# Kernel optimization log

Measured on AMD Instinct MI355X. Metric: run time of the kernel, lower is better.

## Reference

```python
import jax, jax.numpy as jnp
import numpy as np

N = 20000      # nodes
E = 320000     # edges (before self-loops)
G = 64         # graphs in batch
IN = 128       # input_dim
HID = 64       # hidden_dim
H1 = 4         # heads of conv1
NEG_SLOPE = 0.2


def setup_inputs() -> dict:
    key = jax.random.key(0)
    ks = jax.random.split(key, 14)
    x = jax.random.normal(ks[0], (N, IN), jnp.float32)
    edge_index = jax.random.randint(ks[1], (2, E), 0, N, dtype=jnp.int32)
    batch = jnp.sort(jax.random.randint(ks[2], (N,), 0, G, dtype=jnp.int32))
    # conv1: in=IN, out=HID, heads=4, concat
    W1 = jax.random.normal(ks[3], (IN, H1 * HID), jnp.float32) / np.float32(np.sqrt(IN))
    a_src1 = jax.random.normal(ks[4], (H1, HID), jnp.float32) / np.float32(np.sqrt(HID))
    a_dst1 = jax.random.normal(ks[5], (H1, HID), jnp.float32) / np.float32(np.sqrt(HID))
    b1 = jnp.zeros((H1 * HID,), jnp.float32)
    # conv2: in=4*HID, out=HID, heads=1
    W2 = jax.random.normal(ks[6], (H1 * HID, HID), jnp.float32) / np.float32(np.sqrt(H1 * HID))
    a_src2 = jax.random.normal(ks[7], (1, HID), jnp.float32) / np.float32(np.sqrt(HID))
    a_dst2 = jax.random.normal(ks[8], (1, HID), jnp.float32) / np.float32(np.sqrt(HID))
    b2 = jnp.zeros((HID,), jnp.float32)
    # final linear HID -> 1
    W_lin = jax.random.normal(ks[9], (HID, 1), jnp.float32) / np.float32(np.sqrt(HID))
    b_lin = jnp.zeros((1,), jnp.float32)
    return dict(x=x, edge_index=edge_index, batch=batch,
                W1=W1, a_src1=a_src1, a_dst1=a_dst1, b1=b1,
                W2=W2, a_src2=a_src2, a_dst2=a_dst2, b2=b2,
                W_lin=W_lin, b_lin=b_lin)


def gat_conv(x, src, dst, W, a_src, a_dst, b, heads, out_ch, n_nodes):
    """PyG-style GATConv (v1), concat=True, with self-loops already in src/dst."""
    h = (x @ W).reshape(n_nodes, heads, out_ch)          # [N,H,C]
    s = jnp.einsum('nhc,hc->nh', h, a_src)               # [N,H] per-node src score
    d = jnp.einsum('nhc,hc->nh', h, a_dst)               # [N,H] per-node dst score
    logits = jax.nn.leaky_relu(s[src] + d[dst], NEG_SLOPE)   # [Etot,H]
    # segment softmax over incoming edges of each destination node
    m = jax.ops.segment_max(logits, dst, num_segments=n_nodes)
    m = jnp.where(jnp.isfinite(m), m, 0.0)
    e = jnp.exp(logits - m[dst])                         # [Etot,H]
    denom = jax.ops.segment_sum(e, dst, num_segments=n_nodes)
    alpha = e / denom[dst]                               # every node has a self-loop -> denom>0
    out = jax.ops.segment_sum(alpha[:, :, None] * h[src], dst, num_segments=n_nodes)  # [N,H,C]
    return out.reshape(n_nodes, heads * out_ch) + b


def reference(x, edge_index, batch,
              W1, a_src1, a_dst1, b1,
              W2, a_src2, a_dst2, b2,
              W_lin, b_lin):
    n = x.shape[0]
    loop = jnp.arange(n, dtype=edge_index.dtype)
    src = jnp.concatenate([edge_index[0], loop])   # add self-loops (PyG default)
    dst = jnp.concatenate([edge_index[1], loop])
    h = jax.nn.elu(gat_conv(x, src, dst, W1, a_src1, a_dst1, b1, H1, HID, n))
    h = jax.nn.elu(gat_conv(h, src, dst, W2, a_src2, a_dst2, b2, 1, HID, n))
    # global mean pool over graphs
    sums = jax.ops.segment_sum(h, batch, num_segments=G)                 # [G,HID]
    cnt = jax.ops.segment_sum(jnp.ones((n,), h.dtype), batch, num_segments=G)
    pooled = sums / jnp.maximum(cnt, 1.0)[:, None]
    return (pooled @ W_lin + b_lin).squeeze(-1)    # [G]
```

## Files before the change

kernel.cpp:

```cpp
#include <hip/hip_runtime.h>
#include <cstdint>


__device__ __forceinline__ float leaky02(float x) { return x > 0.f ? x : 0.2f * x; }
__device__ __forceinline__ float eluf(float x) { return x > 0.f ? x : expm1f(x); }

template <int H>
__device__ __forceinline__ void sgemm_scores_body(
    const float* __restrict__ A, const float* __restrict__ B, float* __restrict__ C,
    int M, int K, const float* __restrict__ asrc, const float* __restrict__ adst,
    float* __restrict__ sT, float* __restrict__ dS, float* __restrict__ wself,
    int bx, int by, float* As_, float* Bs_) {
    constexpr int Nc = H * 64;
    float (*As)[68] = (float(*)[68])As_;
    float (*Bs)[68] = (float(*)[68])Bs_;
    const int tid = threadIdx.x;
    const int bm = bx * 64, bn = by * 64;
    const int ty = tid >> 4, tx = tid & 15;
    float acc[4][4] = {};
    for (int k0 = 0; k0 < K; k0 += 32) {
#pragma unroll
        for (int i = 0; i < 8; i++) {
            int idx = tid + i * 256;
            int m = idx >> 5, kk = idx & 31;
            int gm = bm + m;
            if (gm >= M) gm = 0;
            As[kk][m] = A[(size_t)gm * K + k0 + kk];
        }
#pragma unroll
        for (int i = 0; i < 8; i++) {
            int idx = tid + i * 256;
            int kk = idx >> 6, n = idx & 63;
            Bs[kk][n] = B[(size_t)(k0 + kk) * Nc + bn + n];
        }
        __syncthreads();
#pragma unroll
        for (int kk = 0; kk < 32; kk++) {
            float4 a4 = *(const float4*)&As[kk][ty * 4];
            float4 b4 = *(const float4*)&Bs[kk][tx * 4];
            float av[4] = {a4.x, a4.y, a4.z, a4.w};
            float bv[4] = {b4.x, b4.y, b4.z, b4.w};
#pragma unroll
            for (int r = 0; r < 4; r++)
#pragma unroll
                for (int c2 = 0; c2 < 4; c2++) acc[r][c2] += av[r] * bv[c2];
        }
        __syncthreads();
    }
    const int h = by;
    float sr[4], dr[4];
#pragma unroll
    for (int r = 0; r < 4; r++) {
        float s = 0.f, d = 0.f;
#pragma unroll
        for (int c2 = 0; c2 < 4; c2++) {
            float hv = acc[r][c2];
            s += hv * asrc[h * 64 + tx * 4 + c2];
            d += hv * adst[h * 64 + tx * 4 + c2];
        }
        sr[r] = s;
        dr[r] = d;
    }
#pragma unroll
    for (int off = 1; off <= 8; off <<= 1) {
#pragma unroll
        for (int r = 0; r < 4; r++) {
            sr[r] += __shfl_xor(sr[r], off);
            dr[r] += __shfl_xor(dr[r], off);
        }
    }
#pragma unroll
    for (int r = 0; r < 4; r++) {
        int gm = bm + ty * 4 + r;
        if (gm < M) {
            float4 o = make_float4(acc[r][0], acc[r][1], acc[r][2], acc[r][3]);
            *(float4*)&C[(size_t)gm * Nc + bn + tx * 4] = o;
            if (tx == 0) {
                sT[(size_t)h * M + gm] = sr[r];
                dS[gm * H + h] = dr[r];
                wself[gm * H + h] = __expf(leaky02(sr[r] + dr[r]));
            }
        }
    }
}

__global__ __launch_bounds__(256) void fused_sgemm4_init_kernel(
    const float* __restrict__ A, const float* __restrict__ B, float* __restrict__ C,
    int M, int K, const float* __restrict__ asrc, const float* __restrict__ adst,
    float* __restrict__ sT, float* __restrict__ dS, float* __restrict__ wself,
    int GBX, int GB1, int4* __restrict__ initp, int colN4, int totN4) {
    __shared__ __align__(16) float As_[32][68];
    __shared__ __align__(16) float Bs_[32][68];
    const int b = blockIdx.x;
    if (b >= GB1) {
        int i = (b - GB1) * 256 + threadIdx.x;
        if (i < totN4)
            initp[i] = (i < colN4) ? make_int4(-1, -1, -1, -1) : make_int4(0, 0, 0, 0);
        return;
    }
    sgemm_scores_body<4>(A, B, C, M, K, asrc, adst, sT, dS, wself,
                         b % GBX, b / GBX, &As_[0][0], &Bs_[0][0]);
}

__global__ __launch_bounds__(256) void sgemm_scores1_kernel(
    const float* __restrict__ A, const float* __restrict__ B, float* __restrict__ C,
    int M, int K, const float* __restrict__ asrc, const float* __restrict__ adst,
    float* __restrict__ sT, float* __restrict__ dS, float* __restrict__ wself) {
    __shared__ __align__(16) float As_[32][68];
    __shared__ __align__(16) float Bs_[32][68];
    sgemm_scores_body<1>(A, B, C, M, K, asrc, adst, sT, dS, wself,
                         blockIdx.x, 0, &As_[0][0], &Bs_[0][0]);
}

__global__ void fill_kernel(const int* __restrict__ src, const int* __restrict__ dst,
                            int* __restrict__ cursor, int* __restrict__ col, int E) {
    int e = blockIdx.x * blockDim.x + threadIdx.x;
    if (e >= E) return;
    int d = dst[e];
    int p = atomicAdd(&cursor[d], 1);
    if (p < 64) col[(d << 6) + p] = src[e];
}

__global__ __launch_bounds__(256) void gat_agg4_kernel(
    const float* __restrict__ hbuf, const float* __restrict__ sT,
    const float* __restrict__ dsc, const float* __restrict__ wself,
    const int* __restrict__ cursor, const int* __restrict__ col,
    const float* __restrict__ bias, float* __restrict__ out, int N) {
    const int slice = blockIdx.x & 7;
    const int lane = threadIdx.x & 63;
    const int cq = lane & 7;
    const int vidx = (blockIdx.x >> 3) * 32 + (threadIdx.x >> 6) * 8 + (lane >> 3);
    const bool valid = vidx < N;
    const int v = min(vidx, N - 1);
    const int deg = min(cursor[v], 64);
    const int base = v << 6;
    const int cbase = slice * 32 + cq * 4;
    const int hh = slice >> 1;
    const float* __restrict__ sTh = sT + (size_t)hh * N;
    const char* __restrict__ hb = (const char*)hbuf + ((size_t)cbase << 2);
    const float dvh = dsc[v * 4 + hh];
    float w = wself[v * 4 + hh];
    float den = w;
    float4 hv = *(const float4*)(hb + ((unsigned)v << 10));
    float4 acc = make_float4(w * hv.x, w * hv.y, w * hv.z, w * hv.w);
    const int end8 = (deg + 7) & ~7;
    for (int j = 0; j < end8; j += 8) {
        int4 a = *(const int4*)&col[base + j];
        int4 b = *(const int4*)&col[base + j + 4];
        unsigned o0 = (unsigned)max(a.x, 0) << 10, o1 = (unsigned)max(a.y, 0) << 10;
        unsigned o2 = (unsigned)max(a.z, 0) << 10, o3 = (unsigned)max(a.w, 0) << 10;
        unsigned o4 = (unsigned)max(b.x, 0) << 10, o5 = (unsigned)max(b.y, 0) << 10;
        unsigned o6 = (unsigned)max(b.z, 0) << 10, o7 = (unsigned)max(b.w, 0) << 10;
        float4 h0 = *(const float4*)(hb + o0);
        float4 h1 = *(const float4*)(hb + o1);
        float4 h2 = *(const float4*)(hb + o2);
        float4 h3 = *(const float4*)(hb + o3);
        float4 h4 = *(const float4*)(hb + o4);
        float4 h5 = *(const float4*)(hb + o5);
        float4 h6 = *(const float4*)(hb + o6);
        float4 h7 = *(const float4*)(hb + o7);
        float w0 = (a.x >= 0) ? __expf(leaky02(sTh[o0 >> 10] + dvh)) : 0.f;
        float w1 = (a.y >= 0) ? __expf(leaky02(sTh[o1 >> 10] + dvh)) : 0.f;
        float w2 = (a.z >= 0) ? __expf(leaky02(sTh[o2 >> 10] + dvh)) : 0.f;
        float w3 = (a.w >= 0) ? __expf(leaky02(sTh[o3 >> 10] + dvh)) : 0.f;
        float w4 = (b.x >= 0) ? __expf(leaky02(sTh[o4 >> 10] + dvh)) : 0.f;
        float w5 = (b.y >= 0) ? __expf(leaky02(sTh[o5 >> 10] + dvh)) : 0.f;
        float w6 = (b.z >= 0) ? __expf(leaky02(sTh[o6 >> 10] + dvh)) : 0.f;
        float w7 = (b.w >= 0) ? __expf(leaky02(sTh[o7 >> 10] + dvh)) : 0.f;
        den += w0 + w1 + w2 + w3 + w4 + w5 + w6 + w7;
        acc.x += w0 * h0.x + w1 * h1.x + w2 * h2.x + w3 * h3.x;
        acc.y += w0 * h0.y + w1 * h1.y + w2 * h2.y + w3 * h3.y;
        acc.z += w0 * h0.z + w1 * h1.z + w2 * h2.z + w3 * h3.z;
        acc.w += w0 * h0.w + w1 * h1.w + w2 * h2.w + w3 * h3.w;
        acc.x += w4 * h4.x + w5 * h5.x + w6 * h6.x + w7 * h7.x;
        acc.y += w4 * h4.y + w5 * h5.y + w6 * h6.y + w7 * h7.y;
        acc.z += w4 * h4.z + w5 * h5.z + w6 * h6.z + w7 * h7.z;
        acc.w += w4 * h4.w + w5 * h5.w + w6 * h6.w + w7 * h7.w;
    }
    if (valid) {
        float4 b4 = *(const float4*)&bias[cbase];
        float inv = 1.f / den;
        float4 r;
        r.x = eluf(acc.x * inv + b4.x);
        r.y = eluf(acc.y * inv + b4.y);
        r.z = eluf(acc.z * inv + b4.z);
        r.w = eluf(acc.w * inv + b4.w);
        *(float4*)&out[(size_t)v * 256 + cbase] = r;
    }
}

__global__ __launch_bounds__(256) void gat_agg1_kernel(
    const float* __restrict__ hbuf, const float* __restrict__ sT,
    const float* __restrict__ dsc, const float* __restrict__ wself,
    const int* __restrict__ cursor, const int* __restrict__ col,
    const float* __restrict__ bias, const float* __restrict__ Wlin,
    float* __restrict__ pn0, float* __restrict__ pn1, int N) {
    const int slice = blockIdx.x & 1;
    const int lane = threadIdx.x & 63;
    const int cq = lane & 7;
    const int vidx = (blockIdx.x >> 1) * 32 + (threadIdx.x >> 6) * 8 + (lane >> 3);
    const bool valid = vidx < N;
    const int v = min(vidx, N - 1);
    const int deg = min(cursor[v], 64);
    const int base = v << 6;
    const int cbase = slice * 32 + cq * 4;
    const char* __restrict__ hb = (const char*)hbuf + ((size_t)cbase << 2);
    const float dv = dsc[v];
    float w = wself[v];
    float den = w;
    float4 hv = *(const float4*)(hb + ((unsigned)v << 8));
    float4 acc = make_float4(w * hv.x, w * hv.y, w * hv.z, w * hv.w);
    const int end8 = (deg + 7) & ~7;
    for (int j = 0; j < end8; j += 8) {
        int4 a = *(const int4*)&col[base + j];
        int4 b = *(const int4*)&col[base + j + 4];
        unsigned i0 = (unsigned)max(a.x, 0), i1 = (unsigned)max(a.y, 0);
        unsigned i2 = (unsigned)max(a.z, 0), i3 = (unsigned)max(a.w, 0);
        unsigned i4 = (unsigned)max(b.x, 0), i5 = (unsigned)max(b.y, 0);
        unsigned i6 = (unsigned)max(b.z, 0), i7 = (unsigned)max(b.w, 0);
        float4 h0 = *(const float4*)(hb + (i0 << 8));
        float4 h1 = *(const float4*)(hb + (i1 << 8));
        float4 h2 = *(const float4*)(hb + (i2 << 8));
        float4 h3 = *(const float4*)(hb + (i3 << 8));
        float4 h4 = *(const float4*)(hb + (i4 << 8));
        float4 h5 = *(const float4*)(hb + (i5 << 8));
        float4 h6 = *(const float4*)(hb + (i6 << 8));
        float4 h7 = *(const float4*)(hb + (i7 << 8));
        float w0 = (a.x >= 0) ? __expf(leaky02(sT[i0] + dv)) : 0.f;
        float w1 = (a.y >= 0) ? __expf(leaky02(sT[i1] + dv)) : 0.f;
        float w2 = (a.z >= 0) ? __expf(leaky02(sT[i2] + dv)) : 0.f;
        float w3 = (a.w >= 0) ? __expf(leaky02(sT[i3] + dv)) : 0.f;
        float w4 = (b.x >= 0) ? __expf(leaky02(sT[i4] + dv)) : 0.f;
        float w5 = (b.y >= 0) ? __expf(leaky02(sT[i5] + dv)) : 0.f;
        float w6 = (b.z >= 0) ? __expf(leaky02(sT[i6] + dv)) : 0.f;
        float w7 = (b.w >= 0) ? __expf(leaky02(sT[i7] + dv)) : 0.f;
        den += w0 + w1 + w2 + w3 + w4 + w5 + w6 + w7;
        acc.x += w0 * h0.x + w1 * h1.x + w2 * h2.x + w3 * h3.x;
        acc.y += w0 * h0.y + w1 * h1.y + w2 * h2.y + w3 * h3.y;
        acc.z += w0 * h0.z + w1 * h1.z + w2 * h2.z + w3 * h3.z;
        acc.w += w0 * h0.w + w1 * h1.w + w2 * h2.w + w3 * h3.w;
        acc.x += w4 * h4.x + w5 * h5.x + w6 * h6.x + w7 * h7.x;
        acc.y += w4 * h4.y + w5 * h5.y + w6 * h6.y + w7 * h7.y;
        acc.z += w4 * h4.z + w5 * h5.z + w6 * h6.z + w7 * h7.z;
        acc.w += w4 * h4.w + w5 * h5.w + w6 * h6.w + w7 * h7.w;
    }
    float4 b4 = *(const float4*)&bias[cbase];
    float4 wl = *(const float4*)&Wlin[cbase];
    float inv = 1.f / den;
    float p = eluf(acc.x * inv + b4.x) * wl.x + eluf(acc.y * inv + b4.y) * wl.y +
              eluf(acc.z * inv + b4.z) * wl.z + eluf(acc.w * inv + b4.w) * wl.w;
    p += __shfl_xor(p, 1);
    p += __shfl_xor(p, 2);
    p += __shfl_xor(p, 4);
    if (valid && cq == 0) (slice ? pn1 : pn0)[v] = p;
}

__global__ __launch_bounds__(64) void finalize_kernel(const float* __restrict__ pn0,
                                                      const float* __restrict__ pn1,
                                                      const int* __restrict__ batch,
                                                      const float* __restrict__ blin,
                                                      float* __restrict__ outp, int N, int G) {
    const int g = blockIdx.x;
    const int lane = threadIdx.x;
    int lo = 0, hi = N;
    while (lo < hi) { int mid = (lo + hi) >> 1; if (batch[mid] < g) lo = mid + 1; else hi = mid; }
    int lo2 = lo, hi2 = N;
    while (lo2 < hi2) { int mid = (lo2 + hi2) >> 1; if (batch[mid] < g + 1) lo2 = mid + 1; else hi2 = mid; }
    float s = 0.f;
    for (int i = lo + lane; i < hi2; i += 64) s += pn0[i] + pn1[i];
#pragma unroll
    for (int off = 32; off > 0; off >>= 1) s += __shfl_xor(s, off);
    if (lane == 0) {
        float cnt = (float)(hi2 - lo);
        outp[g] = s / fmaxf(cnt, 1.f) + blin[0];
    }
}

extern "C" void kernel_launch(void* const* d_in, const int* in_sizes, int n_in,
                              void* d_out, int out_size, void* d_ws, size_t ws_size,
                              hipStream_t stream) {
    const float* x      = (const float*)d_in[0];
    const int*   ei     = (const int*)d_in[1];
    const int*   batch  = (const int*)d_in[2];
    const float* W1     = (const float*)d_in[3];
    const float* a_src1 = (const float*)d_in[4];
    const float* a_dst1 = (const float*)d_in[5];
    const float* b1     = (const float*)d_in[6];
    const float* W2     = (const float*)d_in[7];
    const float* a_src2 = (const float*)d_in[8];
    const float* a_dst2 = (const float*)d_in[9];
    const float* b2     = (const float*)d_in[10];
    const float* Wlin   = (const float*)d_in[11];
    const float* blin   = (const float*)d_in[12];

    const int N = in_sizes[2];
    const int E = in_sizes[1] / 2;
    const int G = out_size;
    const int* src = ei;
    const int* dst = ei + E;

    char* ws = (char*)d_ws;
    size_t off = 0;
    auto carve = [&](size_t bytes) -> char* {
        char* p = ws + off;
        off = (off + bytes + 255) & ~(size_t)255;
        return p;
    };
    float* h1      = (float*)carve((size_t)N * 256 * 4);
    float* out1    = (float*)carve((size_t)N * 256 * 4);
    float* sT1     = (float*)carve((size_t)4 * N * 4);
    float* d1      = (float*)carve((size_t)N * 4 * 4);
    float* wself1  = (float*)carve((size_t)N * 4 * 4);
    float* sT2     = (float*)carve((size_t)N * 4);
    float* d2      = (float*)carve((size_t)N * 4);
    float* wself2  = (float*)carve((size_t)N * 4);
    int*   colcur  = (int*)carve(((size_t)N * 64 + N) * 4);
    float* pn0     = (float*)carve((size_t)N * 4);
    float* pn1     = (float*)carve((size_t)N * 4);
    float* h2      = h1;
    int* col = colcur;
    int* cursor = colcur + (size_t)N * 64;

    const int GBX = (N + 63) / 64;
    const int GB1 = GBX * 4;
    const int totN4 = (N * 64 + N) / 4;
    const int colN4 = N * 16;
    const int GBI = (totN4 + 255) / 256;

    fused_sgemm4_init_kernel<<<GB1 + GBI, 256, 0, stream>>>(
        x, W1, h1, N, 128, a_src1, a_dst1, sT1, d1, wself1,
        GBX, GB1, (int4*)colcur, colN4, totN4);
    fill_kernel<<<(E + 255) / 256, 256, 0, stream>>>(src, dst, cursor, col, E);

    const int nodeGroups32 = (N + 31) / 32;
    gat_agg4_kernel<<<8 * nodeGroups32, 256, 0, stream>>>(h1, sT1, d1, wself1, cursor, col,
                                                          b1, out1, N);
    sgemm_scores1_kernel<<<dim3(GBX, 1), 256, 0, stream>>>(
        out1, W2, h2, N, 256, a_src2, a_dst2, sT2, d2, wself2);
    gat_agg1_kernel<<<2 * nodeGroups32, 256, 0, stream>>>(h2, sT2, d2, wself2, cursor, col,
                                                          b2, Wlin, pn0, pn1, N);
    finalize_kernel<<<G, 64, 0, stream>>>(pn0, pn1, batch, blin, (float*)d_out, N, G);
}
```

Measured before the change: 135.7 us.

## Precompute per-edge layer-1 attention weights in CSR fill kernel

The adjacency-fill kernel now also computes exp(leaky_relu(s_src+d_dst)) for all four heads of every edge and stores it in a slot-aligned, per-head buffer. The layer-1 aggregation then reads these weights contiguously instead of gathering source scores and recomputing exponentials in every channel slice. Source scores are stored node-major so the fill kernel can read them as float4. Both aggregation loops are also reduced from 8-way to 4-way unrolling. The trade-off is an extra scattered write of weights and a larger workspace, plus less memory-level parallelism in the inner loops.

New measurement: 143.2 us. +5.5%, slower.

```diff
diff --git a/kernel.cpp b/kernel.cpp
--- a/kernel.cpp
+++ b/kernel.cpp
@@ -9,7 +9,7 @@
 __device__ __forceinline__ void sgemm_scores_body(
     const float* __restrict__ A, const float* __restrict__ B, float* __restrict__ C,
     int M, int K, const float* __restrict__ asrc, const float* __restrict__ adst,
-    float* __restrict__ sT, float* __restrict__ dS, float* __restrict__ wself,
+    float* __restrict__ sS, float* __restrict__ dS, float* __restrict__ wself,
     int bx, int by, float* As_, float* Bs_) {
     constexpr int Nc = H * 64;
     float (*As)[68] = (float(*)[68])As_;
@@ -76,7 +76,7 @@
             float4 o = make_float4(acc[r][0], acc[r][1], acc[r][2], acc[r][3]);
             *(float4*)&C[(size_t)gm * Nc + bn + tx * 4] = o;
             if (tx == 0) {
-                sT[(size_t)h * M + gm] = sr[r];
+                sS[gm * H + h] = sr[r];
                 dS[gm * H + h] = dr[r];
                 wself[gm * H + h] = __expf(leaky02(sr[r] + dr[r]));
             }
@@ -87,7 +87,7 @@
 __global__ __launch_bounds__(256) void fused_sgemm4_init_kernel(
     const float* __restrict__ A, const float* __restrict__ B, float* __restrict__ C,
     int M, int K, const float* __restrict__ asrc, const float* __restrict__ adst,
-    float* __restrict__ sT, float* __restrict__ dS, float* __restrict__ wself,
+    float* __restrict__ sS, float* __restrict__ dS, float* __restrict__ wself,
     int GBX, int GB1, int4* __restrict__ initp, int colN4, int totN4) {
     __shared__ __align__(16) float As_[32][68];
     __shared__ __align__(16) float Bs_[32][68];
@@ -98,34 +98,44 @@
             initp[i] = (i < colN4) ? make_int4(-1, -1, -1, -1) : make_int4(0, 0, 0, 0);
         return;
     }
-    sgemm_scores_body<4>(A, B, C, M, K, asrc, adst, sT, dS, wself,
+    sgemm_scores_body<4>(A, B, C, M, K, asrc, adst, sS, dS, wself,
                          b % GBX, b / GBX, &As_[0][0], &Bs_[0][0]);
 }
 
 __global__ __launch_bounds__(256) void sgemm_scores1_kernel(
     const float* __restrict__ A, const float* __restrict__ B, float* __restrict__ C,
     int M, int K, const float* __restrict__ asrc, const float* __restrict__ adst,
-    float* __restrict__ sT, float* __restrict__ dS, float* __restrict__ wself) {
+    float* __restrict__ sS, float* __restrict__ dS, float* __restrict__ wself) {
     __shared__ __align__(16) float As_[32][68];
     __shared__ __align__(16) float Bs_[32][68];
-    sgemm_scores_body<1>(A, B, C, M, K, asrc, adst, sT, dS, wself,
+    sgemm_scores_body<1>(A, B, C, M, K, asrc, adst, sS, dS, wself,
                          blockIdx.x, 0, &As_[0][0], &Bs_[0][0]);
 }
 
-__global__ void fill_kernel(const int* __restrict__ src, const int* __restrict__ dst,
-                            int* __restrict__ cursor, int* __restrict__ col, int E) {
+__global__ void fill_w4_kernel(const int* __restrict__ src, const int* __restrict__ dst,
+                               int* __restrict__ cursor, int* __restrict__ col,
+                               const float* __restrict__ s1, const float* __restrict__ d1,
+                               float* __restrict__ w, int E, int N64) {
     int e = blockIdx.x * blockDim.x + threadIdx.x;
     if (e >= E) return;
-    int d = dst[e];
+    int s = src[e], d = dst[e];
     int p = atomicAdd(&cursor[d], 1);
-    if (p < 64) col[(d << 6) + p] = src[e];
+    if (p >= 64) return;
+    int slot = (d << 6) + p;
+    col[slot] = s;
+    float4 sv = *(const float4*)&s1[s * 4];
+    float4 dv = *(const float4*)&d1[d * 4];
+    w[slot]            = __expf(leaky02(sv.x + dv.x));
+    w[N64 + slot]      = __expf(leaky02(sv.y + dv.y));
+    w[2 * N64 + slot]  = __expf(leaky02(sv.z + dv.z));
+    w[3 * N64 + slot]  = __expf(leaky02(sv.w + dv.w));
 }
 
 __global__ __launch_bounds__(256) void gat_agg4_kernel(
-    const float* __restrict__ hbuf, const float* __restrict__ sT,
-    const float* __restrict__ dsc, const float* __restrict__ wself,
-    const int* __restrict__ cursor, const int* __restrict__ col,
-    const float* __restrict__ bias, float* __restrict__ out, int N) {
+    const float* __restrict__ hbuf, const float* __restrict__ w,
+    const float* __restrict__ wself, const int* __restrict__ cursor,
+    const int* __restrict__ col, const float* __restrict__ bias,
+    float* __restrict__ out, int N) {
     const int slice = blockIdx.x & 7;
     const int lane = threadIdx.x & 63;
     const int cq = lane & 7;
@@ -136,46 +146,31 @@
     const int base = v << 6;
     const int cbase = slice * 32 + cq * 4;
     const int hh = slice >> 1;
-    const float* __restrict__ sTh = sT + (size_t)hh * N;
+    const float* __restrict__ wp = w + (size_t)hh * (N << 6);
     const char* __restrict__ hb = (const char*)hbuf + ((size_t)cbase << 2);
-    const float dvh = dsc[v * 4 + hh];
-    float w = wself[v * 4 + hh];
-    float den = w;
+    float ws = wself[v * 4 + hh];
+    float den = ws;
     float4 hv = *(const float4*)(hb + ((unsigned)v << 10));
-    float4 acc = make_float4(w * hv.x, w * hv.y, w * hv.z, w * hv.w);
-    const int end8 = (deg + 7) & ~7;
-    for (int j = 0; j < end8; j += 8) {
-        int4 a = *(const int4*)&col[base + j];
-        int4 b = *(const int4*)&col[base + j + 4];
-        unsigned o0 = (unsigned)max(a.x, 0) << 10, o1 = (unsigned)max(a.y, 0) << 10;
-        unsigned o2 = (unsigned)max(a.z, 0) << 10, o3 = (unsigned)max(a.w, 0) << 10;
-        unsigned o4 = (unsigned)max(b.x, 0) << 10, o5 = (unsigned)max(b.y, 0) << 10;
-        unsigned o6 = (unsigned)max(b.z, 0) << 10, o7 = (unsigned)max(b.w, 0) << 10;
+    float4 acc = make_float4(ws * hv.x, ws * hv.y, ws * hv.z, ws * hv.w);
+    const int end4 = (deg + 3) & ~3;
+    for (int j = 0; j < end4; j += 4) {
+        int4 c4 = *(const int4*)&col[base + j];
+        float4 w4 = *(const float4*)&wp[base + j];
+        unsigned o0 = (unsigned)max(c4.x, 0) << 10, o1 = (unsigned)max(c4.y, 0) << 10;
+        unsigned o2 = (unsigned)max(c4.z, 0) << 10, o3 = (unsigned)max(c4.w, 0) << 10;
         float4 h0 = *(const float4*)(hb + o0);
         float4 h1 = *(const float4*)(hb + o1);
         float4 h2 = *(const float4*)(hb + o2);
         float4 h3 = *(const float4*)(hb + o3);
-        float4 h4 = *(const float4*)(hb + o4);
-        float4 h5 = *(const float4*)(hb + o5);
-        float4 h6 = *(const float4*)(hb + o6);
-        float4 h7 = *(const float4*)(hb + o7);
-        float w0 = (a.x >= 0) ? __expf(leaky02(sTh[o0 >> 10] + dvh)) : 0.f;
-        float w1 = (a.y >= 0) ? __expf(leaky02(sTh[o1 >> 10] + dvh)) : 0.f;
-        float w2 = (a.z >= 0) ? __expf(leaky02(sTh[o2 >> 10] + dvh)) : 0.f;
-        float w3 = (a.w >= 0) ? __expf(leaky02(sTh[o3 >> 10] + dvh)) : 0.f;
-        float w4 = (b.x >= 0) ? __expf(leaky02(sTh[o4 >> 10] + dvh)) : 0.f;
-        float w5 = (b.y >= 0) ? __expf(leaky02(sTh[o5 >> 10] + dvh)) : 0.f;
-        float w6 = (b.z >= 0) ? __expf(leaky02(sTh[o6 >> 10] + dvh)) : 0.f;
-        float w7 = (b.w >= 0) ? __expf(leaky02(sTh[o7 >> 10] + dvh)) : 0.f;
-        den += w0 + w1 + w2 + w3 + w4 + w5 + w6 + w7;
+        float w0 = (c4.x >= 0) ? w4.x : 0.f;
+        float w1 = (c4.y >= 0) ? w4.y : 0.f;
+        float w2 = (c4.z >= 0) ? w4.z : 0.f;
+        float w3 = (c4.w >= 0) ? w4.w : 0.f;
+        den += w0 + w1 + w2 + w3;
         acc.x += w0 * h0.x + w1 * h1.x + w2 * h2.x + w3 * h3.x;
         acc.y += w0 * h0.y + w1 * h1.y + w2 * h2.y + w3 * h3.y;
         acc.z += w0 * h0.z + w1 * h1.z + w2 * h2.z + w3 * h3.z;
         acc.w += w0 * h0.w + w1 * h1.w + w2 * h2.w + w3 * h3.w;
-        acc.x += w4 * h4.x + w5 * h5.x + w6 * h6.x + w7 * h7.x;
-        acc.y += w4 * h4.y + w5 * h5.y + w6 * h6.y + w7 * h7.y;
-        acc.z += w4 * h4.z + w5 * h5.z + w6 * h6.z + w7 * h7.z;
-        acc.w += w4 * h4.w + w5 * h5.w + w6 * h6.w + w7 * h7.w;
     }
     if (valid) {
         float4 b4 = *(const float4*)&bias[cbase];
@@ -190,7 +185,7 @@
 }
 
 __global__ __launch_bounds__(256) void gat_agg1_kernel(
-    const float* __restrict__ hbuf, const float* __restrict__ sT,
+    const float* __restrict__ hbuf, const float* __restrict__ s2,
     const float* __restrict__ dsc, const float* __restrict__ wself,
     const int* __restrict__ cursor, const int* __restrict__ col,
     const float* __restrict__ bias, const float* __restrict__ Wlin,
@@ -206,43 +201,28 @@
     const int cbase = slice * 32 + cq * 4;
     const char* __restrict__ hb = (const char*)hbuf + ((size_t)cbase << 2);
     const float dv = dsc[v];
-    float w = wself[v];
-    float den = w;
+    float ws = wself[v];
+    float den = ws;
     float4 hv = *(const float4*)(hb + ((unsigned)v << 8));
-    float4 acc = make_float4(w * hv.x, w * hv.y, w * hv.z, w * hv.w);
-    const int end8 = (deg + 7) & ~7;
-    for (int j = 0; j < end8; j += 8) {
-        int4 a = *(const int4*)&col[base + j];
-        int4 b = *(const int4*)&col[base + j + 4];
-        unsigned i0 = (unsigned)max(a.x, 0), i1 = (unsigned)max(a.y, 0);
-        unsigned i2 = (unsigned)max(a.z, 0), i3 = (unsigned)max(a.w, 0);
-        unsigned i4 = (unsigned)max(b.x, 0), i5 = (unsigned)max(b.y, 0);
-        unsigned i6 = (unsigned)max(b.z, 0), i7 = (unsigned)max(b.w, 0);
+    float4 acc = make_float4(ws * hv.x, ws * hv.y, ws * hv.z, ws * hv.w);
+    const int end4 = (deg + 3) & ~3;
+    for (int j = 0; j < end4; j += 4) {
+        int4 c4 = *(const int4*)&col[base + j];
+        unsigned i0 = (unsigned)max(c4.x, 0), i1 = (unsigned)max(c4.y, 0);
+        unsigned i2 = (unsigned)max(c4.z, 0), i3 = (unsigned)max(c4.w, 0);
         float4 h0 = *(const float4*)(hb + (i0 << 8));
         float4 h1 = *(const float4*)(hb + (i1 << 8));
         float4 h2 = *(const float4*)(hb + (i2 << 8));
         float4 h3 = *(const float4*)(hb + (i3 << 8));
-        float4 h4 = *(const float4*)(hb + (i4 << 8));
-        float4 h5 = *(const float4*)(hb + (i5 << 8));
-        float4 h6 = *(const float4*)(hb + (i6 << 8));
-        float4 h7 = *(const float4*)(hb + (i7 << 8));
-        float w0 = (a.x >= 0) ? __expf(leaky02(sT[i0] + dv)) : 0.f;
-        float w1 = (a.y >= 0) ? __expf(leaky02(sT[i1] + dv)) : 0.f;
-        float w2 = (a.z >= 0) ? __expf(leaky02(sT[i2] + dv)) : 0.f;
-        float w3 = (a.w >= 0) ? __expf(leaky02(sT[i3] + dv)) : 0.f;
-        float w4 = (b.x >= 0) ? __expf(leaky02(sT[i4] + dv)) : 0.f;
-        float w5 = (b.y >= 0) ? __expf(leaky02(sT[i5] + dv)) : 0.f;
-        float w6 = (b.z >= 0) ? __expf(leaky02(sT[i6] + dv)) : 0.f;
-        float w7 = (b.w >= 0) ? __expf(leaky02(sT[i7] + dv)) : 0.f;
-        den += w0 + w1 + w2 + w3 + w4 + w5 + w6 + w7;
+        float w0 = (c4.x >= 0) ? __expf(leaky02(s2[i0] + dv)) : 0.f;
+        float w1 = (c4.y >= 0) ? __expf(leaky02(s2[i1] + dv)) : 0.f;
+        float w2 = (c4.z >= 0) ? __expf(leaky02(s2[i2] + dv)) : 0.f;
+        float w3 = (c4.w >= 0) ? __expf(leaky02(s2[i3] + dv)) : 0.f;
+        den += w0 + w1 + w2 + w3;
         acc.x += w0 * h0.x + w1 * h1.x + w2 * h2.x + w3 * h3.x;
         acc.y += w0 * h0.y + w1 * h1.y + w2 * h2.y + w3 * h3.y;
         acc.z += w0 * h0.z + w1 * h1.z + w2 * h2.z + w3 * h3.z;
         acc.w += w0 * h0.w + w1 * h1.w + w2 * h2.w + w3 * h3.w;
-        acc.x += w4 * h4.x + w5 * h5.x + w6 * h6.x + w7 * h7.x;
-        acc.y += w4 * h4.y + w5 * h5.y + w6 * h6.y + w7 * h7.y;
-        acc.z += w4 * h4.z + w5 * h5.z + w6 * h6.z + w7 * h7.z;
-        acc.w += w4 * h4.w + w5 * h5.w + w6 * h6.w + w7 * h7.w;
     }
     float4 b4 = *(const float4*)&bias[cbase];
     float4 wl = *(const float4*)&Wlin[cbase];
@@ -308,18 +288,20 @@
     };
     float* h1      = (float*)carve((size_t)N * 256 * 4);
     float* out1    = (float*)carve((size_t)N * 256 * 4);
-    float* sT1     = (float*)carve((size_t)4 * N * 4);
+    float* s1      = (float*)carve((size_t)N * 4 * 4);
     float* d1      = (float*)carve((size_t)N * 4 * 4);
     float* wself1  = (float*)carve((size_t)N * 4 * 4);
-    float* sT2     = (float*)carve((size_t)N * 4);
+    float* s2      = (float*)carve((size_t)N * 4);
     float* d2      = (float*)carve((size_t)N * 4);
     float* wself2  = (float*)carve((size_t)N * 4);
     int*   colcur  = (int*)carve(((size_t)N * 64 + N) * 4);
+    float* wpl     = (float*)carve((size_t)4 * N * 64 * 4);
     float* pn0     = (float*)carve((size_t)N * 4);
     float* pn1     = (float*)carve((size_t)N * 4);
     float* h2      = h1;
     int* col = colcur;
     int* cursor = colcur + (size_t)N * 64;
+    const int N64 = N << 6;
 
     const int GBX = (N + 63) / 64;
     const int GB1 = GBX * 4;
@@ -328,16 +310,16 @@
     const int GBI = (totN4 + 255) / 256;
 
     fused_sgemm4_init_kernel<<<GB1 + GBI, 256, 0, stream>>>(
-        x, W1, h1, N, 128, a_src1, a_dst1, sT1, d1, wself1,
+        x, W1, h1, N, 128, a_src1, a_dst1, s1, d1, wself1,
         GBX, GB1, (int4*)colcur, colN4, totN4);
-    fill_kernel<<<(E + 255) / 256, 256, 0, stream>>>(src, dst, cursor, col, E);
-
+    fill_w4_kernel<<<(E + 255) / 256, 256, 0, stream>>>(src, dst, cursor, col,
+                                                        s1, d1, wpl, E, N64);
     const int nodeGroups32 = (N + 31) / 32;
-    gat_agg4_kernel<<<8 * nodeGroups32, 256, 0, stream>>>(h1, sT1, d1, wself1, cursor, col,
+    gat_agg4_kernel<<<8 * nodeGroups32, 256, 0, stream>>>(h1, wpl, wself1, cursor, col,
                                                           b1, out1, N);
     sgemm_scores1_kernel<<<dim3(GBX, 1), 256, 0, stream>>>(
-        out1, W2, h2, N, 256, a_src2, a_dst2, sT2, d2, wself2);
-    gat_agg1_kernel<<<2 * nodeGroups32, 256, 0, stream>>>(h2, sT2, d2, wself2, cursor, col,
+        out1, W2, h2, N, 256, a_src2, a_dst2, s2, d2, wself2);
+    gat_agg1_kernel<<<2 * nodeGroups32, 256, 0, stream>>>(h2, s2, d2, wself2, cursor, col,
                                                           b2, Wlin, pn0, pn1, N);
     finalize_kernel<<<G, 64, 0, stream>>>(pn0, pn1, batch, blin, (float*)d_out, N, G);
 }
```
